# Performance work log

Hardware: AMD Instinct MI355X
Metric: run time of the kernel (lower is better)

Reference implementation:

```python
import jax, jax.numpy as jnp
import numpy as np

DIM = 1024
NUM_HEADS = 16
HEAD_DIM = DIM // NUM_HEADS
B, N_Q, N_KV = 8, 1024, 1024


def setup_inputs() -> dict:
    key = jax.random.key(0)
    ks = jax.random.split(key, 12)
    s = 1.0 / np.sqrt(DIM)
    inp = {
        "query": jax.random.normal(ks[0], (B, N_Q, DIM), jnp.float32),
        "key_value": jax.random.normal(ks[1], (B, N_KV, DIM), jnp.float32),
        "cluster_matrix": jax.random.normal(ks[2], (B, N_Q, N_KV), jnp.float32),
        "Wq": jax.random.uniform(ks[3], (DIM, DIM), jnp.float32, -s, s),
        "bq": jax.random.uniform(ks[4], (DIM,), jnp.float32, -s, s),
        "Wk": jax.random.uniform(ks[5], (DIM, DIM), jnp.float32, -s, s),
        "bk": jax.random.uniform(ks[6], (DIM,), jnp.float32, -s, s),
        "Wv": jax.random.uniform(ks[7], (DIM, DIM), jnp.float32, -s, s),
        "bv": jax.random.uniform(ks[8], (DIM,), jnp.float32, -s, s),
        "Wo": jax.random.uniform(ks[9], (DIM, DIM), jnp.float32, -s, s),
        "bo": jax.random.uniform(ks[10], (DIM,), jnp.float32, -s, s),
    }
    return inp


def reference(query, key_value, cluster_matrix, Wq, bq, Wk, bk, Wv, bv, Wo, bo):
    Bsz, Nq, D = query.shape
    Nkv = key_value.shape[1]
    H, Hd = NUM_HEADS, HEAD_DIM
    # projections (torch Linear: x @ W.T + b)
    Q = (query @ Wq.T + bq).reshape(Bsz, Nq, H, Hd).transpose(0, 2, 1, 3)      # [B,H,Nq,Hd]
    K = (key_value @ Wk.T + bk).reshape(Bsz, Nkv, H, Hd).transpose(0, 2, 1, 3)  # [B,H,Nkv,Hd]
    V = (key_value @ Wv.T + bv).reshape(Bsz, Nkv, H, Hd).transpose(0, 2, 1, 3)
    scale = 1.0 / jnp.sqrt(jnp.asarray(Hd, Q.dtype))
    scores = jnp.einsum("bhqd,bhkd->bhqk", Q, K) * scale + cluster_matrix[:, None]  # [B,H,Nq,Nkv]
    attn_weights = jax.nn.softmax(scores, axis=-1)
    attn_out = jnp.einsum("bhqk,bhkd->bhqd", attn_weights, V)
    attn_out = attn_out.transpose(0, 2, 1, 3).reshape(Bsz, Nq, D)
    updated_query = attn_out @ Wo.T + bo
    attn_matrix = attn_weights.mean(axis=1)  # head-mean [B,Nq,Nkv]
    return updated_query, attn_matrix
```

## Files before the change

### kernel.cpp

```cpp
#include <hip/hip_runtime.h>
#include <stdint.h>
#include <stddef.h>

typedef __attribute__((ext_vector_type(4))) float  f32x4;
typedef __attribute__((ext_vector_type(4))) float  float4v;
typedef __attribute__((ext_vector_type(8))) short  s16x8;
typedef __attribute__((ext_vector_type(4))) short  s16x4;
typedef __attribute__((ext_vector_type(2))) unsigned int u32x2;

#define DEV static __device__ __forceinline__

DEV short f2bf(float f) {
  unsigned u = __builtin_bit_cast(unsigned, f);
  u = u + 0x7fffu + ((u >> 16) & 1u);
  return (short)(u >> 16);
}
DEV float bf2f(short s) {
  unsigned u = ((unsigned)(unsigned short)s) << 16;
  return __builtin_bit_cast(float, u);
}
DEV f32x4 vmax4(f32x4 a, f32x4 b) {
  f32x4 r;
  r[0] = fmaxf(a[0], b[0]); r[1] = fmaxf(a[1], b[1]);
  r[2] = fmaxf(a[2], b[2]); r[3] = fmaxf(a[3], b[3]);
  return r;
}
DEV void gload16(const void* g, void* l) {
  __builtin_amdgcn_global_load_lds((const __attribute__((address_space(1))) void*)g,
                                   (__attribute__((address_space(3))) void*)l, 16, 0, 0);
}

__global__ void cvt4(const float4v* __restrict__ src, s16x4* __restrict__ dst, int n4) {
  int i = blockIdx.x * 256 + threadIdx.x;
  if (i >= n4) return;
  float4v v = src[i];
  s16x4 o; o.x = f2bf(v.x); o.y = f2bf(v.y); o.z = f2bf(v.z); o.w = f2bf(v.w);
  dst[i] = o;
}
__global__ void cvt_dup(const float4v* __restrict__ src, s16x8* __restrict__ dst, int n4) {
  int i = blockIdx.x * 256 + threadIdx.x;
  if (i >= n4) return;
  float4v v = src[i];
  s16x8 o;
  o[0] = f2bf(v.x); o[1] = o[0];
  o[2] = f2bf(v.y); o[3] = o[2];
  o[4] = f2bf(v.z); o[5] = o[4];
  o[6] = f2bf(v.w); o[7] = o[6];
  dst[i] = o;
}

template <int EPI, int KDIM>
__global__ __launch_bounds__(256) void gemm_nt(const short* __restrict__ A,
                                               const short* __restrict__ Bw,
                                               const float* __restrict__ bias,
                                               void* __restrict__ Cp) {
  __shared__ __attribute__((aligned(16))) short As[2][128 * 32];
  __shared__ __attribute__((aligned(16))) short Bs[2][128 * 32];
  const int tid = threadIdx.x;
  const int wg  = blockIdx.x;
  const int swz = (wg & 7) * ((int)gridDim.x >> 3) + (wg >> 3);
  const int bm = swz >> 3, bn = swz & 7;
  const int mbase = bm * 128, nbase = bn * 128;
  const int w = tid >> 6, l = tid & 63;
  const int wm = w >> 1, wn = w & 1;

  auto stage = [&](int buf, int kt) {
#pragma unroll
    for (int j = 0; j < 2; ++j) {
      int cb  = w * 128 + j * 64;
      int ci  = cb + l;
      int row = ci >> 2, cc = ci & 3;
      int c   = cc ^ ((row >> 1) & 3);
      gload16(A  + (size_t)(mbase + row) * KDIM + kt * 32 + c * 8, &As[buf][cb * 8]);
      gload16(Bw + (size_t)(nbase + row) * KDIM + kt * 32 + c * 8, &Bs[buf][cb * 8]);
    }
  };

  f32x4 acc[4][4];
#pragma unroll
  for (int i = 0; i < 4; ++i)
#pragma unroll
    for (int j = 0; j < 4; ++j) acc[i][j] = (f32x4){0.f, 0.f, 0.f, 0.f};

  const int KSTEPS = KDIM / 32;
  stage(0, 0);
  for (int kt = 0; kt < KSTEPS; ++kt) {
    __syncthreads();
    if (kt + 1 < KSTEPS) stage((kt + 1) & 1, kt + 1);
    const int buf = kt & 1;
    s16x8 af[4], bf[4];
    const int g = l >> 4;
#pragma unroll
    for (int i = 0; i < 4; ++i) {
      int ra = wm * 64 + i * 16 + (l & 15);
      int pa = g ^ ((ra >> 1) & 3);
      af[i] = *(const s16x8*)&As[buf][ra * 32 + pa * 8];
      int rb = wn * 64 + i * 16 + (l & 15);
      int pb = g ^ ((rb >> 1) & 3);
      bf[i] = *(const s16x8*)&Bs[buf][rb * 32 + pb * 8];
    }
#pragma unroll
    for (int i = 0; i < 4; ++i)
#pragma unroll
      for (int j = 0; j < 4; ++j)
        acc[i][j] = __builtin_amdgcn_mfma_f32_16x16x32_bf16(af[i], bf[j], acc[i][j], 0, 0, 0);
  }

  float bj[4];
#pragma unroll
  for (int j = 0; j < 4; ++j) bj[j] = bias[nbase + wn * 64 + j * 16 + (l & 15)];
#pragma unroll
  for (int i = 0; i < 4; ++i) {
#pragma unroll
    for (int j = 0; j < 4; ++j) {
      int m0 = mbase + wm * 64 + i * 16 + (l >> 4) * 4;
      int n  = nbase + wn * 64 + j * 16 + (l & 15);
      if constexpr (EPI == 0) {
        short* C16 = (short*)Cp;
#pragma unroll
        for (int jj = 0; jj < 4; ++jj)
          C16[(size_t)(m0 + jj) * 1024 + n] = f2bf(acc[i][j][jj] + bj[j]);
      } else if constexpr (EPI == 1) {
        float* Cf = (float*)Cp;
#pragma unroll
        for (int jj = 0; jj < 4; ++jj)
          Cf[(size_t)(m0 + jj) * 1024 + n] = acc[i][j][jj] + bj[j];
      } else {
        short* C16 = (short*)Cp;
        int bb = m0 >> 10, kv = m0 & 1023;
        s16x4 o;
#pragma unroll
        for (int jj = 0; jj < 4; ++jj) o[jj] = f2bf(acc[i][j][jj] + bj[j]);
        *(s16x4*)&C16[((size_t)(bb * 1024 + n)) * 1024 + kv] = o;
      }
    }
  }
}

__global__ __launch_bounds__(512, 2) void attn_fused2(const short* __restrict__ Qp,
                                                      const short* __restrict__ Kp,
                                                      const short* __restrict__ Vt,
                                                      const float* __restrict__ cluster,
                                                      short* __restrict__ AO2,
                                                      float* __restrict__ Amean) {
  constexpr int PSTR = 1032;
  __shared__ __attribute__((aligned(16))) short Pbuf[32 * PSTR];
  __shared__ float mlbuf[32][8][2];
  const int tid = threadIdx.x;
  const int b = blockIdx.y, qt = blockIdx.x;
  const int w = tid >> 6, l = tid & 63;
  const int li = l & 15, g = l >> 4;
  const int wkv = w * 128;
  const int qb = w >> 2, db = w & 3;
  const float scale = 0.125f;
  const float LOG2E = 1.4426950408889634f;

  const size_t qrow0 = (size_t)(b * 1024 + qt * 32);
  const size_t krow0 = (size_t)(b * 1024);

  float macc[2][8][4];
#pragma unroll
  for (int a = 0; a < 2; ++a)
#pragma unroll
    for (int kb = 0; kb < 8; ++kb)
#pragma unroll
      for (int jj = 0; jj < 4; ++jj) macc[a][kb][jj] = 0.f;

  for (int h = 0; h < 16; ++h) {
    s16x8 qf[2][2];
#pragma unroll
    for (int qcb = 0; qcb < 2; ++qcb)
#pragma unroll
      for (int kc = 0; kc < 2; ++kc)
        qf[qcb][kc] = *(const s16x8*)&Qp[(qrow0 + qcb * 16 + li) * 1024 + h * 64 + kc * 32 + g * 8];

    f32x4 acc[2][8];
#pragma unroll
    for (int a = 0; a < 2; ++a)
#pragma unroll
      for (int kb = 0; kb < 8; ++kb) acc[a][kb] = (f32x4){0.f, 0.f, 0.f, 0.f};

#pragma unroll
    for (int half = 0; half < 2; ++half) {
      s16x8 kf[8];
#pragma unroll
      for (int i = 0; i < 8; ++i) {
        int kb = half * 4 + (i >> 1), kc = i & 1;
        kf[i] = *(const s16x8*)&Kp[(krow0 + wkv + kb * 16 + li) * 1024 + h * 64 + kc * 32 + g * 8];
      }
#pragma unroll
      for (int i = 0; i < 8; ++i) {
        int kb = half * 4 + (i >> 1), kc = i & 1;
#pragma unroll
        for (int qcb = 0; qcb < 2; ++qcb)
          acc[qcb][kb] = __builtin_amdgcn_mfma_f32_16x16x32_bf16(kf[i], qf[qcb][kc], acc[qcb][kb], 0, 0, 0);
      }
    }

    float mw[2], lw[2];
#pragma unroll
    for (int qcb = 0; qcb < 2; ++qcb) {
      const float* clp = cluster + (qrow0 + qcb * 16 + li) * 1024 + wkv + 4 * g;
#pragma unroll
      for (int kb = 0; kb < 8; ++kb) {
        f32x4 cl = *(const f32x4*)(clp + kb * 16);
        acc[qcb][kb] = acc[qcb][kb] * scale + cl;
      }
      f32x4 mx = acc[qcb][0];
#pragma unroll
      for (int kb = 1; kb < 8; ++kb) mx = vmax4(mx, acc[qcb][kb]);
      float m = fmaxf(fmaxf(mx[0], mx[1]), fmaxf(mx[2], mx[3]));
      m = fmaxf(m, __shfl_xor(m, 16, 64));
      m = fmaxf(m, __shfl_xor(m, 32, 64));
      f32x4 s4 = (f32x4){0.f, 0.f, 0.f, 0.f};
#pragma unroll
      for (int kb = 0; kb < 8; ++kb) {
        f32x4 e;
#pragma unroll
        for (int jj = 0; jj < 4; ++jj) e[jj] = __builtin_amdgcn_exp2f((acc[qcb][kb][jj] - m) * LOG2E);
        acc[qcb][kb] = e;
        s4 += e;
      }
      float s = (s4[0] + s4[1]) + (s4[2] + s4[3]);
      s += __shfl_xor(s, 16, 64);
      s += __shfl_xor(s, 32, 64);
      mw[qcb] = m; lw[qcb] = s;
    }
    if (l < 16) {
#pragma unroll
      for (int qcb = 0; qcb < 2; ++qcb) {
        mlbuf[qcb * 16 + l][w][0] = mw[qcb];
        mlbuf[qcb * 16 + l][w][1] = lw[qcb];
      }
    }
    __syncthreads();

#pragma unroll
    for (int qcb = 0; qcb < 2; ++qcb) {
      const int q = qcb * 16 + li;
      float m = mlbuf[q][0][0];
#pragma unroll
      for (int j = 1; j < 8; ++j) m = fmaxf(m, mlbuf[q][j][0]);
      float lt = 0.f;
#pragma unroll
      for (int j = 0; j < 8; ++j) lt += mlbuf[q][j][1] * __builtin_amdgcn_exp2f((mlbuf[q][j][0] - m) * LOG2E);
      const float c = __builtin_amdgcn_exp2f((mw[qcb] - m) * LOG2E) / lt;
#pragma unroll
      for (int kb = 0; kb < 8; ++kb) {
        f32x4 p = acc[qcb][kb] * c;
#pragma unroll
        for (int jj = 0; jj < 4; ++jj) macc[qcb][kb][jj] += p[jj];
        unsigned u0 = (unsigned)(unsigned short)f2bf(p[0]) | ((unsigned)(unsigned short)f2bf(p[1]) << 16);
        unsigned u1 = (unsigned)(unsigned short)f2bf(p[2]) | ((unsigned)(unsigned short)f2bf(p[3]) << 16);
        u32x2 uu; uu[0] = u0; uu[1] = u1;
        *(u32x2*)&Pbuf[q * PSTR + wkv + kb * 16 + 4 * g] = uu;
      }
    }
    __syncthreads();

    f32x4 o0 = (f32x4){0.f,0.f,0.f,0.f}, o1 = o0, o2 = o0, o3 = o0;
    const short* vbase = Vt + ((size_t)((b * 16 + h) * 64 + db * 16 + li)) * 1024 + g * 8;
    const short* pbase = &Pbuf[(qb * 16 + li) * PSTR + g * 8];
#pragma unroll
    for (int kc = 0; kc < 32; kc += 4) {
      s16x8 pf0 = *(const s16x8*)(pbase + (kc + 0) * 32);
      s16x8 vf0 = *(const s16x8*)(vbase + (kc + 0) * 32);
      s16x8 pf1 = *(const s16x8*)(pbase + (kc + 1) * 32);
      s16x8 vf1 = *(const s16x8*)(vbase + (kc + 1) * 32);
      s16x8 pf2 = *(const s16x8*)(pbase + (kc + 2) * 32);
      s16x8 vf2 = *(const s16x8*)(vbase + (kc + 2) * 32);
      s16x8 pf3 = *(const s16x8*)(pbase + (kc + 3) * 32);
      s16x8 vf3 = *(const s16x8*)(vbase + (kc + 3) * 32);
      o0 = __builtin_amdgcn_mfma_f32_16x16x32_bf16(pf0, vf0, o0, 0, 0, 0);
      o1 = __builtin_amdgcn_mfma_f32_16x16x32_bf16(pf1, vf1, o1, 0, 0, 0);
      o2 = __builtin_amdgcn_mfma_f32_16x16x32_bf16(pf2, vf2, o2, 0, 0, 0);
      o3 = __builtin_amdgcn_mfma_f32_16x16x32_bf16(pf3, vf3, o3, 0, 0, 0);
    }
    f32x4 of = (o0 + o1) + (o2 + o3);
#pragma unroll
    for (int jj = 0; jj < 4; ++jj) {
      int q = qb * 16 + g * 4 + jj;
      int d = db * 16 + li;
      float x = of[jj];
      short hi = f2bf(x);
      short lo = f2bf(x - bf2f(hi));
      *(unsigned*)&AO2[(qrow0 + q) * 2048 + (size_t)(h * 64 + d) * 2] =
          (unsigned)(unsigned short)hi | ((unsigned)(unsigned short)lo << 16);
    }
  }

#pragma unroll
  for (int qcb = 0; qcb < 2; ++qcb)
#pragma unroll
    for (int kb = 0; kb < 8; ++kb) {
      f32x4 v;
#pragma unroll
      for (int jj = 0; jj < 4; ++jj) v[jj] = macc[qcb][kb][jj] * 0.0625f;
      *(f32x4*)&Amean[(qrow0 + qcb * 16 + li) * 1024 + wkv + kb * 16 + 4 * g] = v;
    }
}

extern "C" void kernel_launch(void* const* d_in, const int* in_sizes, int n_in,
                              void* d_out, int out_size, void* d_ws, size_t ws_size,
                              hipStream_t stream) {
  (void)in_sizes; (void)n_in; (void)out_size; (void)ws_size;
  const float* query     = (const float*)d_in[0];
  const float* key_value = (const float*)d_in[1];
  const float* cluster   = (const float*)d_in[2];
  const float* Wq = (const float*)d_in[3];
  const float* bq = (const float*)d_in[4];
  const float* Wk = (const float*)d_in[5];
  const float* bk = (const float*)d_in[6];
  const float* Wv = (const float*)d_in[7];
  const float* bv = (const float*)d_in[8];
  const float* Wo = (const float*)d_in[9];
  const float* bo = (const float*)d_in[10];

  char* ws = (char*)d_ws;
  short* qb  = (short*)(ws);
  short* kvb = (short*)(ws + 16777216);
  short* Wqb = (short*)(ws + 33554432);
  short* Wkb = (short*)(ws + 35651584);
  short* Wvb = (short*)(ws + 37748736);
  short* Wo2 = (short*)(ws + 39845888);
  short* Qp  = (short*)(ws + 44040192);
  short* Kp  = (short*)(ws + 60817408);
  short* Vtp = (short*)(ws + 77594624);
  short* AO2 = (short*)(ws + 94371840);

  float* out_uq = (float*)d_out;
  float* out_am = (float*)d_out + 8388608;

  cvt4<<<8192, 256, 0, stream>>>((const float4v*)query,     (s16x4*)qb,  2097152);
  cvt4<<<8192, 256, 0, stream>>>((const float4v*)key_value, (s16x4*)kvb, 2097152);
  cvt4<<<1024, 256, 0, stream>>>((const float4v*)Wq, (s16x4*)Wqb, 262144);
  cvt4<<<1024, 256, 0, stream>>>((const float4v*)Wk, (s16x4*)Wkb, 262144);
  cvt4<<<1024, 256, 0, stream>>>((const float4v*)Wv, (s16x4*)Wvb, 262144);
  cvt_dup<<<1024, 256, 0, stream>>>((const float4v*)Wo, (s16x8*)Wo2, 262144);

  gemm_nt<0, 1024><<<512, 256, 0, stream>>>(qb,  Wqb, bq, Qp);
  gemm_nt<0, 1024><<<512, 256, 0, stream>>>(kvb, Wkb, bk, Kp);
  gemm_nt<2, 1024><<<512, 256, 0, stream>>>(kvb, Wvb, bv, Vtp);

  attn_fused2<<<dim3(32, 8), 512, 0, stream>>>(Qp, Kp, Vtp, cluster, AO2, out_am);

  gemm_nt<1, 2048><<<512, 256, 0, stream>>>(AO2, Wo2, bo, out_uq);
}
```

Baseline: 551.1 us.

## Hoist cluster bias out of head loop and split PV over KV halves

Cluster bias is loaded once per block and pre-scaled by log2e, rather than reloaded for each of 16 heads, and the softmax scale is folded into an exp2 base. The PV matmul is reorganized so each wave covers both query blocks over half the KV range, reusing each V fragment twice, with a cross-wave reduction through a small LDS buffer and an extra barrier. This aims to cut global cluster traffic and V loads, at the cost of more registers (cluster values held across heads) and one more sync per head.

```diff
diff --git a/kernel.cpp b/kernel.cpp
--- a/kernel.cpp
+++ b/kernel.cpp
@@ -137,7 +137,7 @@
   }
 }
 
-__global__ __launch_bounds__(512, 2) void attn_fused2(const short* __restrict__ Qp,
+__global__ __launch_bounds__(512, 2) void attn_fused3(const short* __restrict__ Qp,
                                                       const short* __restrict__ Kp,
                                                       const short* __restrict__ Vt,
                                                       const float* __restrict__ cluster,
@@ -145,26 +145,31 @@
                                                       float* __restrict__ Amean) {
   constexpr int PSTR = 1032;
   __shared__ __attribute__((aligned(16))) short Pbuf[32 * PSTR];
-  __shared__ float mlbuf[32][8][2];
+  __shared__ float mlbuf[32][20];
+  __shared__ __attribute__((aligned(16))) f32x4 obuf[4][2][16][4];
   const int tid = threadIdx.x;
   const int b = blockIdx.y, qt = blockIdx.x;
   const int w = tid >> 6, l = tid & 63;
   const int li = l & 15, g = l >> 4;
   const int wkv = w * 128;
-  const int qb = w >> 2, db = w & 3;
-  const float scale = 0.125f;
+  const int db = w & 3, kvh = w >> 2;
   const float LOG2E = 1.4426950408889634f;
+  const float scaleL = 0.125f * LOG2E;
 
   const size_t qrow0 = (size_t)(b * 1024 + qt * 32);
   const size_t krow0 = (size_t)(b * 1024);
 
-  float macc[2][8][4];
-#pragma unroll
-  for (int a = 0; a < 2; ++a)
-#pragma unroll
-    for (int kb = 0; kb < 8; ++kb)
-#pragma unroll
-      for (int jj = 0; jj < 4; ++jj) macc[a][kb][jj] = 0.f;
+  f32x4 clv[2][8], macc[2][8];
+#pragma unroll
+  for (int qcb = 0; qcb < 2; ++qcb) {
+    const float* clp = cluster + (qrow0 + qcb * 16 + li) * 1024 + wkv + 4 * g;
+#pragma unroll
+    for (int kb = 0; kb < 8; ++kb) {
+      f32x4 cl = *(const f32x4*)(clp + kb * 16);
+      clv[qcb][kb] = cl * LOG2E;
+      macc[qcb][kb] = (f32x4){0.f, 0.f, 0.f, 0.f};
+    }
+  }
 
   for (int h = 0; h < 16; ++h) {
     s16x8 qf[2][2];
@@ -181,16 +186,16 @@
       for (int kb = 0; kb < 8; ++kb) acc[a][kb] = (f32x4){0.f, 0.f, 0.f, 0.f};
 
 #pragma unroll
-    for (int half = 0; half < 2; ++half) {
-      s16x8 kf[8];
-#pragma unroll
-      for (int i = 0; i < 8; ++i) {
-        int kb = half * 4 + (i >> 1), kc = i & 1;
+    for (int quarter = 0; quarter < 4; ++quarter) {
+      s16x8 kf[4];
+#pragma unroll
+      for (int i = 0; i < 4; ++i) {
+        int kb = quarter * 2 + (i >> 1), kc = i & 1;
         kf[i] = *(const s16x8*)&Kp[(krow0 + wkv + kb * 16 + li) * 1024 + h * 64 + kc * 32 + g * 8];
       }
 #pragma unroll
-      for (int i = 0; i < 8; ++i) {
-        int kb = half * 4 + (i >> 1), kc = i & 1;
+      for (int i = 0; i < 4; ++i) {
+        int kb = quarter * 2 + (i >> 1), kc = i & 1;
 #pragma unroll
         for (int qcb = 0; qcb < 2; ++qcb)
           acc[qcb][kb] = __builtin_amdgcn_mfma_f32_16x16x32_bf16(kf[i], qf[qcb][kc], acc[qcb][kb], 0, 0, 0);
@@ -200,12 +205,9 @@
     float mw[2], lw[2];
 #pragma unroll
     for (int qcb = 0; qcb < 2; ++qcb) {
-      const float* clp = cluster + (qrow0 + qcb * 16 + li) * 1024 + wkv + 4 * g;
-#pragma unroll
-      for (int kb = 0; kb < 8; ++kb) {
-        f32x4 cl = *(const f32x4*)(clp + kb * 16);
-        acc[qcb][kb] = acc[qcb][kb] * scale + cl;
-      }
+#pragma unroll
+      for (int kb = 0; kb < 8; ++kb)
+        acc[qcb][kb] = acc[qcb][kb] * scaleL + clv[qcb][kb];
       f32x4 mx = acc[qcb][0];
 #pragma unroll
       for (int kb = 1; kb < 8; ++kb) mx = vmax4(mx, acc[qcb][kb]);
@@ -217,7 +219,7 @@
       for (int kb = 0; kb < 8; ++kb) {
         f32x4 e;
 #pragma unroll
-        for (int jj = 0; jj < 4; ++jj) e[jj] = __builtin_amdgcn_exp2f((acc[qcb][kb][jj] - m) * LOG2E);
+        for (int jj = 0; jj < 4; ++jj) e[jj] = __builtin_amdgcn_exp2f(acc[qcb][kb][jj] - m);
         acc[qcb][kb] = e;
         s4 += e;
       }
@@ -229,8 +231,8 @@
     if (l < 16) {
 #pragma unroll
       for (int qcb = 0; qcb < 2; ++qcb) {
-        mlbuf[qcb * 16 + l][w][0] = mw[qcb];
-        mlbuf[qcb * 16 + l][w][1] = lw[qcb];
+        mlbuf[qcb * 16 + l][2 * w]     = mw[qcb];
+        mlbuf[qcb * 16 + l][2 * w + 1] = lw[qcb];
       }
     }
     __syncthreads();
@@ -238,18 +240,17 @@
 #pragma unroll
     for (int qcb = 0; qcb < 2; ++qcb) {
       const int q = qcb * 16 + li;
-      float m = mlbuf[q][0][0];
-#pragma unroll
-      for (int j = 1; j < 8; ++j) m = fmaxf(m, mlbuf[q][j][0]);
+      float m = mlbuf[q][0];
+#pragma unroll
+      for (int j = 1; j < 8; ++j) m = fmaxf(m, mlbuf[q][2 * j]);
       float lt = 0.f;
 #pragma unroll
-      for (int j = 0; j < 8; ++j) lt += mlbuf[q][j][1] * __builtin_amdgcn_exp2f((mlbuf[q][j][0] - m) * LOG2E);
-      const float c = __builtin_amdgcn_exp2f((mw[qcb] - m) * LOG2E) / lt;
+      for (int j = 0; j < 8; ++j) lt += mlbuf[q][2 * j + 1] * __builtin_amdgcn_exp2f(mlbuf[q][2 * j] - m);
+      const float c = __builtin_amdgcn_exp2f(mw[qcb] - m) / lt;
 #pragma unroll
       for (int kb = 0; kb < 8; ++kb) {
         f32x4 p = acc[qcb][kb] * c;
-#pragma unroll
-        for (int jj = 0; jj < 4; ++jj) macc[qcb][kb][jj] += p[jj];
+        macc[qcb][kb] += p;
         unsigned u0 = (unsigned)(unsigned short)f2bf(p[0]) | ((unsigned)(unsigned short)f2bf(p[1]) << 16);
         unsigned u1 = (unsigned)(unsigned short)f2bf(p[2]) | ((unsigned)(unsigned short)f2bf(p[3]) << 16);
         u32x2 uu; uu[0] = u0; uu[1] = u1;
@@ -258,46 +259,50 @@
     }
     __syncthreads();
 
-    f32x4 o0 = (f32x4){0.f,0.f,0.f,0.f}, o1 = o0, o2 = o0, o3 = o0;
-    const short* vbase = Vt + ((size_t)((b * 16 + h) * 64 + db * 16 + li)) * 1024 + g * 8;
-    const short* pbase = &Pbuf[(qb * 16 + li) * PSTR + g * 8];
-#pragma unroll
-    for (int kc = 0; kc < 32; kc += 4) {
-      s16x8 pf0 = *(const s16x8*)(pbase + (kc + 0) * 32);
-      s16x8 vf0 = *(const s16x8*)(vbase + (kc + 0) * 32);
-      s16x8 pf1 = *(const s16x8*)(pbase + (kc + 1) * 32);
-      s16x8 vf1 = *(const s16x8*)(vbase + (kc + 1) * 32);
-      s16x8 pf2 = *(const s16x8*)(pbase + (kc + 2) * 32);
-      s16x8 vf2 = *(const s16x8*)(vbase + (kc + 2) * 32);
-      s16x8 pf3 = *(const s16x8*)(pbase + (kc + 3) * 32);
-      s16x8 vf3 = *(const s16x8*)(vbase + (kc + 3) * 32);
-      o0 = __builtin_amdgcn_mfma_f32_16x16x32_bf16(pf0, vf0, o0, 0, 0, 0);
-      o1 = __builtin_amdgcn_mfma_f32_16x16x32_bf16(pf1, vf1, o1, 0, 0, 0);
-      o2 = __builtin_amdgcn_mfma_f32_16x16x32_bf16(pf2, vf2, o2, 0, 0, 0);
-      o3 = __builtin_amdgcn_mfma_f32_16x16x32_bf16(pf3, vf3, o3, 0, 0, 0);
-    }
-    f32x4 of = (o0 + o1) + (o2 + o3);
-#pragma unroll
-    for (int jj = 0; jj < 4; ++jj) {
-      int q = qb * 16 + g * 4 + jj;
-      int d = db * 16 + li;
-      float x = of[jj];
-      short hi = f2bf(x);
-      short lo = f2bf(x - bf2f(hi));
-      *(unsigned*)&AO2[(qrow0 + q) * 2048 + (size_t)(h * 64 + d) * 2] =
-          (unsigned)(unsigned short)hi | ((unsigned)(unsigned short)lo << 16);
+    f32x4 o0a = (f32x4){0.f,0.f,0.f,0.f}, o0b = o0a, o1a = o0a, o1b = o0a;
+    {
+      const short* vb = Vt + ((size_t)((b * 16 + h) * 64 + db * 16 + li)) * 1024 + kvh * 512 + g * 8;
+      const short* p0 = &Pbuf[li * PSTR + kvh * 512 + g * 8];
+      const short* p1 = &Pbuf[(16 + li) * PSTR + kvh * 512 + g * 8];
+#pragma unroll
+      for (int kc = 0; kc < 16; kc += 2) {
+        s16x8 vfa = *(const s16x8*)(vb + kc * 32);
+        s16x8 vfb = *(const s16x8*)(vb + kc * 32 + 32);
+        s16x8 pa0 = *(const s16x8*)(p0 + kc * 32);
+        s16x8 pb0 = *(const s16x8*)(p0 + kc * 32 + 32);
+        s16x8 pa1 = *(const s16x8*)(p1 + kc * 32);
+        s16x8 pb1 = *(const s16x8*)(p1 + kc * 32 + 32);
+        o0a = __builtin_amdgcn_mfma_f32_16x16x32_bf16(pa0, vfa, o0a, 0, 0, 0);
+        o1a = __builtin_amdgcn_mfma_f32_16x16x32_bf16(pa1, vfa, o1a, 0, 0, 0);
+        o0b = __builtin_amdgcn_mfma_f32_16x16x32_bf16(pb0, vfb, o0b, 0, 0, 0);
+        o1b = __builtin_amdgcn_mfma_f32_16x16x32_bf16(pb1, vfb, o1b, 0, 0, 0);
+      }
+    }
+    f32x4 of0 = o0a + o0b, of1 = o1a + o1b;
+    if (kvh == 1) obuf[db][0][li][g] = of0;
+    else          obuf[db][1][li][g] = of1;
+    __syncthreads();
+    {
+      f32x4 of = (kvh == 0) ? (of0 + obuf[db][0][li][g]) : (of1 + obuf[db][1][li][g]);
+      const int qb = kvh;
+#pragma unroll
+      for (int jj = 0; jj < 4; ++jj) {
+        int q = qb * 16 + g * 4 + jj;
+        int d = db * 16 + li;
+        float x = of[jj];
+        short hi = f2bf(x);
+        short lo = f2bf(x - bf2f(hi));
+        *(unsigned*)&AO2[(qrow0 + q) * 2048 + (size_t)(h * 64 + d) * 2] =
+            (unsigned)(unsigned short)hi | ((unsigned)(unsigned short)lo << 16);
+      }
     }
   }
 
 #pragma unroll
   for (int qcb = 0; qcb < 2; ++qcb)
 #pragma unroll
-    for (int kb = 0; kb < 8; ++kb) {
-      f32x4 v;
-#pragma unroll
-      for (int jj = 0; jj < 4; ++jj) v[jj] = macc[qcb][kb][jj] * 0.0625f;
-      *(f32x4*)&Amean[(qrow0 + qcb * 16 + li) * 1024 + wkv + kb * 16 + 4 * g] = v;
-    }
+    for (int kb = 0; kb < 8; ++kb)
+      *(f32x4*)&Amean[(qrow0 + qcb * 16 + li) * 1024 + wkv + kb * 16 + 4 * g] = macc[qcb][kb] * 0.0625f;
 }
 
 extern "C" void kernel_launch(void* const* d_in, const int* in_sizes, int n_in,
@@ -342,7 +347,7 @@
   gemm_nt<0, 1024><<<512, 256, 0, stream>>>(kvb, Wkb, bk, Kp);
   gemm_nt<2, 1024><<<512, 256, 0, stream>>>(kvb, Wvb, bv, Vtp);
 
-  attn_fused2<<<dim3(32, 8), 512, 0, stream>>>(Qp, Kp, Vtp, cluster, AO2, out_am);
+  attn_fused3<<<dim3(32, 8), 512, 0, stream>>>(Qp, Kp, Vtp, cluster, AO2, out_am);
 
   gemm_nt<1, 2048><<<512, 256, 0, stream>>>(AO2, Wo2, bo, out_uq);
 }
```

After: 496.1 us. -10.0%, faster.
